# Performance work log

Hardware: AMD Instinct MI355X
Metric: run time of the kernel (lower is better)

The kernel has to match this reference:

```python
import jax, jax.numpy as jnp
import numpy as np

_BIG = 1e4  # kornia uses 1e4 as the 'infinity' for masked-out kernel positions


def _windows(img, pad_val):
    """Return the 9 shifted 3x3 neighborhoods of img, stacked on axis 0.
    img: [B,C,H,W] -> [9,B,C,H,W]. Border padded with pad_val so padded
    pixels never win the min (erosion) / max (dilation), matching kornia.
    """
    B, C, H, W = img.shape
    p = jnp.pad(img, ((0, 0), (0, 0), (1, 1), (1, 1)), constant_values=pad_val)
    return jnp.stack([p[..., i:i + H, j:j + W]
                      for i in range(3) for j in range(3)], axis=0)


def _erosion(img, mask):
    w = _windows(img, _BIG)
    return jnp.min(jnp.where(mask, w, _BIG), axis=0)


def _dilation(img, mask):
    w = _windows(img, -_BIG)
    return jnp.max(jnp.where(mask, w, -_BIG), axis=0)


def setup_inputs() -> dict:
    key = jax.random.key(0)
    img = jax.random.uniform(key, (8, 3, 1024, 1024), dtype=jnp.float32)
    # kernel0: symmetric 3x3 cross structuring element
    kernel = jnp.array([[0, 1, 0], [1, 1, 1], [0, 1, 0]], dtype=jnp.int32)
    return {"img": img, "kernel": kernel}


def reference(img, kernel):
    # morphological opening = erosion followed by dilation, same structuring element
    mask = (kernel.reshape(9, 1, 1, 1, 1) == 1)
    eroded = _erosion(img, mask)
    opened = _dilation(eroded, mask)
    return opened
```

## Files before the change

kernel.cpp:

```cpp
#include <hip/hip_runtime.h>

#define BIGV 1e4f

constexpr int RH = 16;
constexpr int TY = 4;

struct Row { float2 L; float4 M; float2 R; };
struct Ero { float eL; float4 eM; float eR; };

__device__ __forceinline__ float min3f(float a, float b, float c) { return fminf(fminf(a, b), c); }
__device__ __forceinline__ float max3f(float a, float b, float c) { return fmaxf(fmaxf(a, b), c); }

__device__ __forceinline__ Row load_row(const float* __restrict__ p,
                                        int y, int gx, int H, int W) {
    Row r;
    if (y >= 0 && y < H) {
        const float* q = p + (size_t)y * W;
        r.M = *(const float4*)(q + gx);
        if (gx > 0)      r.L = *(const float2*)(q + gx - 2);
        else             r.L = make_float2(BIGV, BIGV);
        if (gx + 4 < W)  r.R = *(const float2*)(q + gx + 4);
        else             r.R = make_float2(BIGV, BIGV);
    } else {
        r.L = make_float2(BIGV, BIGV);
        r.M = make_float4(BIGV, BIGV, BIGV, BIGV);
        r.R = make_float2(BIGV, BIGV);
    }
    return r;
}

__device__ __forceinline__ float rget(const Row& r, int q) {
    switch (q) {
        case -2: return r.L.x; case -1: return r.L.y;
        case 0:  return r.M.x; case 1:  return r.M.y;
        case 2:  return r.M.z; case 3:  return r.M.w;
        case 4:  return r.R.x; default: return r.R.y;
    }
}
__device__ __forceinline__ float eget(const Ero& e, int q) {
    switch (q) {
        case -1: return e.eL;
        case 0:  return e.eM.x; case 1:  return e.eM.y;
        case 2:  return e.eM.z; case 3:  return e.eM.w;
        default: return e.eR;
    }
}

__device__ __forceinline__ Ero erode_cross(const Row& a, const Row& b, const Row& c,
                                           int r, int H, int gx, int W) {
    Ero e;
    if (r >= 0 && r < H) {
        float vL = min3f(a.L.y, b.L.y, c.L.y);
        float v0 = min3f(a.M.x, b.M.x, c.M.x);
        float v1 = min3f(a.M.y, b.M.y, c.M.y);
        float v2 = min3f(a.M.z, b.M.z, c.M.z);
        float v3 = min3f(a.M.w, b.M.w, c.M.w);
        float vR = min3f(a.R.x, b.R.x, c.R.x);
        e.eL   = min3f(vL, b.L.x, b.M.x);
        e.eM.x = min3f(v0, b.L.y, b.M.y);
        e.eM.y = min3f(v1, b.M.x, b.M.z);
        e.eM.z = min3f(v2, b.M.y, b.M.w);
        e.eM.w = min3f(v3, b.M.z, b.R.x);
        e.eR   = min3f(vR, b.M.w, b.R.y);
        if (gx == 0)     e.eL = -BIGV;
        if (gx + 4 >= W) e.eR = -BIGV;
    } else {
        e.eL = -BIGV; e.eM = make_float4(-BIGV, -BIGV, -BIGV, -BIGV); e.eR = -BIGV;
    }
    return e;
}

__device__ __forceinline__ float4 dilate_cross(const Ero& t, const Ero& m, const Ero& b) {
    float vx = max3f(t.eM.x, m.eM.x, b.eM.x);
    float vy = max3f(t.eM.y, m.eM.y, b.eM.y);
    float vz = max3f(t.eM.z, m.eM.z, b.eM.z);
    float vw = max3f(t.eM.w, m.eM.w, b.eM.w);
    float4 o;
    o.x = max3f(vx, m.eL,   m.eM.y);
    o.y = max3f(vy, m.eM.x, m.eM.z);
    o.z = max3f(vz, m.eM.y, m.eM.w);
    o.w = max3f(vw, m.eM.z, m.eR);
    return o;
}

__device__ __forceinline__ Ero erode_gen(const Row& a, const Row& b, const Row& c,
                                         const bool* m, int r, int H, int gx, int W) {
    Ero e;
    if (r >= 0 && r < H) {
        float v[6];
#pragma unroll
        for (int p = 0; p < 6; ++p) {
            float acc = BIGV;
#pragma unroll
            for (int k = 0; k < 9; ++k) {
                const int di = k / 3, dj = k % 3;
                const Row& rr = (di == 0) ? a : ((di == 1) ? b : c);
                float t = rget(rr, p - 2 + dj);
                acc = fminf(acc, m[k] ? t : BIGV);
            }
            v[p] = acc;
        }
        e.eL = v[0]; e.eM.x = v[1]; e.eM.y = v[2]; e.eM.z = v[3]; e.eM.w = v[4]; e.eR = v[5];
        if (gx == 0)     e.eL = -BIGV;
        if (gx + 4 >= W) e.eR = -BIGV;
    } else {
        e.eL = -BIGV; e.eM = make_float4(-BIGV, -BIGV, -BIGV, -BIGV); e.eR = -BIGV;
    }
    return e;
}

__device__ __forceinline__ float4 dilate_gen(const Ero& e0, const Ero& e1, const Ero& e2,
                                             const bool* m) {
    float o[4];
#pragma unroll
    for (int j = 0; j < 4; ++j) {
        float acc = -BIGV;
#pragma unroll
        for (int k = 0; k < 9; ++k) {
            const int di = k / 3, dj = k % 3;
            const Ero& ee = (di == 0) ? e0 : ((di == 1) ? e1 : e2);
            float t = eget(ee, j + dj - 1);
            acc = fmaxf(acc, m[k] ? t : -BIGV);
        }
        o[j] = acc;
    }
    return make_float4(o[0], o[1], o[2], o[3]);
}

template <bool CROSS>
__device__ __forceinline__ void run(const float* __restrict__ img, float* __restrict__ out,
                                    const bool* m, int gx, int y0, int H, int W) {
    Row B = load_row(img, y0 - 2, gx, H, W);
    Row C = load_row(img, y0 - 1, gx, H, W);
    Row D = load_row(img, y0,     gx, H, W);
    Ero E0 = CROSS ? erode_cross(B, C, D, y0 - 1, H, gx, W)
                   : erode_gen(B, C, D, m, y0 - 1, H, gx, W);
    C = D;
    Row Cc = load_row(img, y0,     gx, H, W);
    Row Dd = load_row(img, y0 + 1, gx, H, W);
    Ero E1 = CROSS ? erode_cross(load_row(img, y0 - 1, gx, H, W), Cc, Dd, y0, H, gx, W)
                   : erode_gen(load_row(img, y0 - 1, gx, H, W), Cc, Dd, m, y0, H, gx, W);
#pragma unroll
    for (int i = 0; i < RH; ++i) {
        const int y = y0 + i;
        Row N = load_row(img, y + 2, gx, H, W);
        Ero E2 = CROSS ? erode_cross(Cc, Dd, N, y + 1, H, gx, W)
                       : erode_gen(Cc, Dd, N, m, y + 1, H, gx, W);
        float4 o = CROSS ? dilate_cross(E0, E1, E2) : dilate_gen(E0, E1, E2, m);
        *(float4*)(out + (size_t)y * W + gx) = o;
        Cc = Dd; Dd = N;
        E0 = E1; E1 = E2;
    }
}

__global__ __launch_bounds__(256) void opening_kernel(
    const float* __restrict__ img, const int* __restrict__ kern,
    float* __restrict__ out, int H, int W)
{
    const int lx = threadIdx.x & 63;
    const int ty = threadIdx.x >> 6;
    const int gx = blockIdx.x * 256 + lx * 4;
    const int y0 = (blockIdx.y * TY + ty) * RH;
    const size_t pbase = (size_t)blockIdx.z * H * W;

    bool m[9];
#pragma unroll
    for (int k = 0; k < 9; ++k) m[k] = (kern[k] == 1);

    const bool cross = m[1] && m[3] && m[4] && m[5] && m[7] &&
                       !m[0] && !m[2] && !m[6] && !m[8];

    if (cross) run<true >(img + pbase, out + pbase, m, gx, y0, H, W);
    else       run<false>(img + pbase, out + pbase, m, gx, y0, H, W);
}

extern "C" void kernel_launch(void* const* d_in, const int* in_sizes, int n_in,
                              void* d_out, int out_size, void* d_ws, size_t ws_size,
                              hipStream_t stream) {
    const float* img  = (const float*)d_in[0];
    const int*   kern = (const int*)d_in[1];
    float*       out  = (float*)d_out;

    const int H = 1024, W = 1024;
    const int planes = in_sizes[0] / (H * W);

    dim3 block(256);
    dim3 grid(W / 256, H / (TY * RH), planes);
    opening_kernel<<<grid, block, 0, stream>>>(img, kern, out, H, W);
}
```

Measured before the change: 183.4 us.

## Use wavefront shuffles for halo columns, prefetch next row, halve rows per thread

Each thread now loads only its own float4 per row. Left and right neighbour columns come from __shfl_up and __shfl_down across the 64-lane wavefront, and only the edge lanes issue the extra float2 global loads. The row loop also prefetches the next input row one iteration ahead, and RH drops from 16 to 8, which doubles the number of blocks but adds more vertical halo overhead per block. The aim is to cut redundant global loads and hide load latency, at the cost of shuffle instructions and extra halo rows.

```diff
diff --git a/kernel.cpp b/kernel.cpp
--- a/kernel.cpp
+++ b/kernel.cpp
@@ -2,31 +2,42 @@
 
 #define BIGV 1e4f
 
-constexpr int RH = 16;
+constexpr int RH = 8;
 constexpr int TY = 4;
 
+struct Raw { float4 M; float2 L; float2 R; };
 struct Row { float2 L; float4 M; float2 R; };
 struct Ero { float eL; float4 eM; float eR; };
 
 __device__ __forceinline__ float min3f(float a, float b, float c) { return fminf(fminf(a, b), c); }
 __device__ __forceinline__ float max3f(float a, float b, float c) { return fmaxf(fmaxf(a, b), c); }
 
-__device__ __forceinline__ Row load_row(const float* __restrict__ p,
-                                        int y, int gx, int H, int W) {
-    Row r;
+__device__ __forceinline__ Raw load_raw(const float* __restrict__ img, int y, int gx,
+                                        int lx, int H, int W) {
+    Raw r;
+    r.L = make_float2(BIGV, BIGV);
+    r.R = make_float2(BIGV, BIGV);
     if (y >= 0 && y < H) {
-        const float* q = p + (size_t)y * W;
+        const float* q = img + (size_t)y * W;
         r.M = *(const float4*)(q + gx);
-        if (gx > 0)      r.L = *(const float2*)(q + gx - 2);
-        else             r.L = make_float2(BIGV, BIGV);
-        if (gx + 4 < W)  r.R = *(const float2*)(q + gx + 4);
-        else             r.R = make_float2(BIGV, BIGV);
+        if (lx == 0  && gx > 0)     r.L = *(const float2*)(q + gx - 2);
+        if (lx == 63 && gx + 4 < W) r.R = *(const float2*)(q + gx + 4);
     } else {
-        r.L = make_float2(BIGV, BIGV);
         r.M = make_float4(BIGV, BIGV, BIGV, BIGV);
-        r.R = make_float2(BIGV, BIGV);
     }
     return r;
+}
+
+__device__ __forceinline__ Row rowify(const Raw& r, int lx) {
+    Row o;
+    o.M = r.M;
+    float lz = __shfl_up(r.M.z, 1, 64);
+    float lw = __shfl_up(r.M.w, 1, 64);
+    float rx = __shfl_down(r.M.x, 1, 64);
+    float ry = __shfl_down(r.M.y, 1, 64);
+    o.L = (lx == 0)  ? r.L : make_float2(lz, lw);
+    o.R = (lx == 63) ? r.R : make_float2(rx, ry);
+    return o;
 }
 
 __device__ __forceinline__ float rget(const Row& r, int q) {
@@ -50,18 +61,12 @@
                                            int r, int H, int gx, int W) {
     Ero e;
     if (r >= 0 && r < H) {
-        float vL = min3f(a.L.y, b.L.y, c.L.y);
-        float v0 = min3f(a.M.x, b.M.x, c.M.x);
-        float v1 = min3f(a.M.y, b.M.y, c.M.y);
-        float v2 = min3f(a.M.z, b.M.z, c.M.z);
-        float v3 = min3f(a.M.w, b.M.w, c.M.w);
-        float vR = min3f(a.R.x, b.R.x, c.R.x);
-        e.eL   = min3f(vL, b.L.x, b.M.x);
-        e.eM.x = min3f(v0, b.L.y, b.M.y);
-        e.eM.y = min3f(v1, b.M.x, b.M.z);
-        e.eM.z = min3f(v2, b.M.y, b.M.w);
-        e.eM.w = min3f(v3, b.M.z, b.R.x);
-        e.eR   = min3f(vR, b.M.w, b.R.y);
+        e.eL   = min3f(min3f(a.L.y, b.L.y, c.L.y), b.L.x, b.M.x);
+        e.eM.x = min3f(min3f(a.M.x, b.M.x, c.M.x), b.L.y, b.M.y);
+        e.eM.y = min3f(min3f(a.M.y, b.M.y, c.M.y), b.M.x, b.M.z);
+        e.eM.z = min3f(min3f(a.M.z, b.M.z, c.M.z), b.M.y, b.M.w);
+        e.eM.w = min3f(min3f(a.M.w, b.M.w, c.M.w), b.M.z, b.R.x);
+        e.eR   = min3f(min3f(a.R.x, b.R.x, c.R.x), b.M.w, b.R.y);
         if (gx == 0)     e.eL = -BIGV;
         if (gx + 4 >= W) e.eR = -BIGV;
     } else {
@@ -71,15 +76,11 @@
 }
 
 __device__ __forceinline__ float4 dilate_cross(const Ero& t, const Ero& m, const Ero& b) {
-    float vx = max3f(t.eM.x, m.eM.x, b.eM.x);
-    float vy = max3f(t.eM.y, m.eM.y, b.eM.y);
-    float vz = max3f(t.eM.z, m.eM.z, b.eM.z);
-    float vw = max3f(t.eM.w, m.eM.w, b.eM.w);
     float4 o;
-    o.x = max3f(vx, m.eL,   m.eM.y);
-    o.y = max3f(vy, m.eM.x, m.eM.z);
-    o.z = max3f(vz, m.eM.y, m.eM.w);
-    o.w = max3f(vw, m.eM.z, m.eR);
+    o.x = max3f(max3f(t.eM.x, m.eM.x, b.eM.x), m.eL,   m.eM.y);
+    o.y = max3f(max3f(t.eM.y, m.eM.y, b.eM.y), m.eM.x, m.eM.z);
+    o.z = max3f(max3f(t.eM.z, m.eM.z, b.eM.z), m.eM.y, m.eM.w);
+    o.w = max3f(max3f(t.eM.w, m.eM.w, b.eM.w), m.eM.z, m.eR);
     return o;
 }
 
@@ -129,27 +130,36 @@
 
 template <bool CROSS>
 __device__ __forceinline__ void run(const float* __restrict__ img, float* __restrict__ out,
-                                    const bool* m, int gx, int y0, int H, int W) {
-    Row B = load_row(img, y0 - 2, gx, H, W);
-    Row C = load_row(img, y0 - 1, gx, H, W);
-    Row D = load_row(img, y0,     gx, H, W);
-    Ero E0 = CROSS ? erode_cross(B, C, D, y0 - 1, H, gx, W)
-                   : erode_gen(B, C, D, m, y0 - 1, H, gx, W);
-    C = D;
-    Row Cc = load_row(img, y0,     gx, H, W);
-    Row Dd = load_row(img, y0 + 1, gx, H, W);
-    Ero E1 = CROSS ? erode_cross(load_row(img, y0 - 1, gx, H, W), Cc, Dd, y0, H, gx, W)
-                   : erode_gen(load_row(img, y0 - 1, gx, H, W), Cc, Dd, m, y0, H, gx, W);
+                                    const bool* m, int gx, int y0, int lx, int H, int W) {
+    Raw rb = load_raw(img, y0 - 2, gx, lx, H, W);
+    Raw rc = load_raw(img, y0 - 1, gx, lx, H, W);
+    Raw rd = load_raw(img, y0,     gx, lx, H, W);
+    Raw re = load_raw(img, y0 + 1, gx, lx, H, W);
+    Raw pref = load_raw(img, y0 + 2, gx, lx, H, W);
+
+    Row B   = rowify(rb, lx);
+    Row C   = rowify(rc, lx);
+    Row Cur = rowify(rd, lx);
+    Ero E0 = CROSS ? erode_cross(B, C, Cur, y0 - 1, H, gx, W)
+                   : erode_gen(B, C, Cur, m, y0 - 1, H, gx, W);
+    Row Nxt = rowify(re, lx);
+    Ero E1 = CROSS ? erode_cross(C, Cur, Nxt, y0, H, gx, W)
+                   : erode_gen(C, Cur, Nxt, m, y0, H, gx, W);
+
 #pragma unroll
     for (int i = 0; i < RH; ++i) {
         const int y = y0 + i;
-        Row N = load_row(img, y + 2, gx, H, W);
-        Ero E2 = CROSS ? erode_cross(Cc, Dd, N, y + 1, H, gx, W)
-                       : erode_gen(Cc, Dd, N, m, y + 1, H, gx, W);
+        Raw pref2 = pref;
+        if (i < RH - 1)
+            pref2 = load_raw(img, y + 3, gx, lx, H, W);
+        Row N = rowify(pref, lx);
+        Ero E2 = CROSS ? erode_cross(Cur, Nxt, N, y + 1, H, gx, W)
+                       : erode_gen(Cur, Nxt, N, m, y + 1, H, gx, W);
         float4 o = CROSS ? dilate_cross(E0, E1, E2) : dilate_gen(E0, E1, E2, m);
         *(float4*)(out + (size_t)y * W + gx) = o;
-        Cc = Dd; Dd = N;
+        Cur = Nxt; Nxt = N;
         E0 = E1; E1 = E2;
+        pref = pref2;
     }
 }
 
@@ -170,8 +180,8 @@
     const bool cross = m[1] && m[3] && m[4] && m[5] && m[7] &&
                        !m[0] && !m[2] && !m[6] && !m[8];
 
-    if (cross) run<true >(img + pbase, out + pbase, m, gx, y0, H, W);
-    else       run<false>(img + pbase, out + pbase, m, gx, y0, H, W);
+    if (cross) run<true >(img + pbase, out + pbase, m, gx, y0, lx, H, W);
+    else       run<false>(img + pbase, out + pbase, m, gx, y0, lx, H, W);
 }
 
 extern "C" void kernel_launch(void* const* d_in, const int* in_sizes, int n_in,
```

Result: faster. 179.7 us (-2.0%).
